# Kernel optimization log

Hardware: AMD Instinct MI355X
Metric: run time of the kernel (lower is better)

The kernel has to match this reference:

```python
import jax, jax.numpy as jnp
import numpy as np

DIM = 1024
DIM_HEADS = 128   # dim_inner
HEADS = 8         # dim_out // dim_heads
DHEAD = DIM_HEADS // HEADS  # = 16, per the Rearrange '(qkv h d)'
EPS = 1e-6


def setup_inputs() -> dict:
    key = jax.random.key(0)
    k1, k2, k3 = jax.random.split(key, 3)
    x = jax.random.normal(k1, (8, 4096, DIM), dtype=jnp.float32)
    norm_weight = jnp.ones((DIM,), dtype=jnp.float32)
    w_qkv = jax.random.normal(k2, (3 * DIM_HEADS, DIM), dtype=jnp.float32) * (1.0 / np.sqrt(DIM))
    temperature = jnp.zeros((HEADS, 1, 1), dtype=jnp.float32)
    w_out = jax.random.normal(k3, (DIM, DIM_HEADS), dtype=jnp.float32) * (1.0 / np.sqrt(DIM_HEADS))
    return {"x": x, "norm_weight": norm_weight, "w_qkv": w_qkv,
            "temperature": temperature, "w_out": w_out}


def _l2norm(t, axis=-1):
    # F.normalize(p=2): divide by max(||t||, eps) with eps=1e-12
    n = jnp.sqrt(jnp.sum(t * t, axis=axis, keepdims=True))
    return t / jnp.maximum(n, 1e-12)


def reference(x, norm_weight, w_qkv, temperature, w_out):
    b, n, _ = x.shape
    # RMSNorm
    ms = jnp.mean(x * x, axis=-1, keepdims=True)
    xn = x * jax.lax.rsqrt(ms + EPS) * norm_weight
    # QKV projection: b n (3 h d) -> 3 b h d n
    qkv = jnp.einsum('bnc,oc->bno', xn, w_qkv)
    qkv = qkv.reshape(b, n, 3, HEADS, DHEAD).transpose(2, 0, 3, 4, 1)  # [3,b,h,d,n]
    q, k, v = qkv[0], qkv[1], qkv[2]
    # l2-normalize along token axis (last axis, n)
    q = _l2norm(q)
    k = _l2norm(k)
    q = q * jnp.exp(temperature)  # (h,1,1) broadcasts over (b,h,d,n)
    # XCiT channel (cross-covariance) attention: d x d similarity over tokens
    sim = jnp.einsum('bhin,bhjn->bhij', q, k)
    attn = jax.nn.softmax(sim, axis=-1)
    out = jnp.einsum('bhij,bhjn->bhin', attn, v)  # [b,h,d,n]
    # b h d n -> b n (h d), then output projection
    out = out.transpose(0, 3, 1, 2).reshape(b, n, HEADS * DHEAD)
    return jnp.einsum('bnc,oc->bno', out, w_out)
```

## Files before the change

### kernel.cpp

```cpp
#include <hip/hip_runtime.h>
#include <hip/hip_bf16.h>
#include <stdint.h>

typedef __bf16 bf16_t;
typedef __bf16 bf16x8 __attribute__((ext_vector_type(8)));
typedef float  f32x4  __attribute__((ext_vector_type(4)));

#define DIM    1024
#define NTOK   4096
#define NB     8
#define ROWS   (NB*NTOK)
#define QKVC   384
#define INNER  128

#define GLD16(g, l) __builtin_amdgcn_global_load_lds( \
    (const __attribute__((address_space(1))) void*)(g), \
    (__attribute__((address_space(3))) void*)(l), 16, 0, 0)

#define OFF_WQ    131072u
#define OFF_QKV   1048576u
#define OFF_STATS 26214400u
#define OFF_ATTN  30932992u
#define OFF_WEFF  30998528u

__global__ __launch_bounds__(256) void k_wconv(const float* __restrict__ wq,
    const float* __restrict__ nw, bf16_t* __restrict__ wqb)
{
    int o = blockIdx.x;
    int c = threadIdx.x * 4;
    float4 wv = *reinterpret_cast<const float4*>(wq + (size_t)o*DIM + c);
    float4 nv = *reinterpret_cast<const float4*>(nw + c);
    bf16_t* dst = wqb + (size_t)o*DIM + c;
    dst[0]=(bf16_t)(wv.x*nv.x); dst[1]=(bf16_t)(wv.y*nv.y);
    dst[2]=(bf16_t)(wv.z*nv.z); dst[3]=(bf16_t)(wv.w*nv.w);
}

__global__ __launch_bounds__(512, 2) void k_qkv_gemm(const float* __restrict__ x,
    const bf16_t* __restrict__ wqb, bf16_t* __restrict__ qkv,
    float* __restrict__ stats)
{
    __shared__ bf16_t Al[2][128*64];
    __shared__ bf16_t Bl[2][384*64];
    __shared__ float srow[128];
    int mt = blockIdx.x;
    int row0 = mt*128;
    int t = threadIdx.x;
    int lane = t & 63, lr = lane & 15, lg = lane >> 4;
    int w = t >> 6, wm = w >> 2, wn = w & 3;

    int rA = t >> 2;
    int fo = (t & 3) * 16;
    const float* xrow = x + (size_t)(row0 + rA)*DIM + fo;
    int ws0 = ((t & 3)*2)     ^ (rA & 7);
    int ws1 = ((t & 3)*2 + 1) ^ (rA & 7);

    int srB = t >> 3;
    int sk8 = ((t & 7) ^ (srB & 7)) * 8;
    const bf16_t* bbase = wqb + (size_t)srB*DIM + sk8;
    int ldsoff = (t & ~63) * 8;

    int rsw = lr & 7;

    float4 u0, u1, u2, u3;

#define LOADA(kt) do {                                                   \
        const float4* _xs = reinterpret_cast<const float4*>(xrow + (kt)*64); \
        u0 = _xs[0]; u1 = _xs[1]; u2 = _xs[2]; u3 = _xs[3];              \
    } while (0)

#define STAGEB(buf, kt) do {                                             \
        int _ko = (kt)*64;                                               \
        _Pragma("unroll")                                                \
        for (int _c = 0; _c < 6; _c++)                                   \
            GLD16(bbase + _ko + (size_t)(64*_c)*DIM,                     \
                  &Bl[buf][ldsoff + _c*4096]);                           \
    } while (0)

#define WRITEA(buf) do {                                                 \
        ssq += u0.x*u0.x + u0.y*u0.y + u0.z*u0.z + u0.w*u0.w             \
             + u1.x*u1.x + u1.y*u1.y + u1.z*u1.z + u1.w*u1.w             \
             + u2.x*u2.x + u2.y*u2.y + u2.z*u2.z + u2.w*u2.w             \
             + u3.x*u3.x + u3.y*u3.y + u3.z*u3.z + u3.w*u3.w;            \
        bf16x8 v0, v1;                                                   \
        v0[0]=(bf16_t)u0.x; v0[1]=(bf16_t)u0.y; v0[2]=(bf16_t)u0.z;      \
        v0[3]=(bf16_t)u0.w; v0[4]=(bf16_t)u1.x; v0[5]=(bf16_t)u1.y;      \
        v0[6]=(bf16_t)u1.z; v0[7]=(bf16_t)u1.w;                          \
        v1[0]=(bf16_t)u2.x; v1[1]=(bf16_t)u2.y; v1[2]=(bf16_t)u2.z;      \
        v1[3]=(bf16_t)u2.w; v1[4]=(bf16_t)u3.x; v1[5]=(bf16_t)u3.y;      \
        v1[6]=(bf16_t)u3.z; v1[7]=(bf16_t)u3.w;                          \
        *reinterpret_cast<bf16x8*>(&Al[buf][rA*64 + ws0*8]) = v0;        \
        *reinterpret_cast<bf16x8*>(&Al[buf][rA*64 + ws1*8]) = v1;        \
    } while (0)

    float ssq = 0.f;
    f32x4 acc[4][6] = {};

    LOADA(0);
    STAGEB(0, 0);
    WRITEA(0);
    __syncthreads();

    for (int kt = 0; kt < 16; kt++) {
        int cur = kt & 1;
        if (kt < 15) {
            LOADA(kt + 1);
            STAGEB(cur ^ 1, kt + 1);
        }
        #pragma unroll
        for (int kk = 0; kk < 2; kk++) {
            int kb = ((kk*4 + lg) ^ rsw) * 8;
            bf16x8 af[4], bfr[6];
            #pragma unroll
            for (int mi = 0; mi < 4; mi++)
                af[mi] = *reinterpret_cast<const bf16x8*>(
                    &Al[cur][(wm*64 + mi*16 + lr)*64 + kb]);
            #pragma unroll
            for (int ni = 0; ni < 6; ni++)
                bfr[ni] = *reinterpret_cast<const bf16x8*>(
                    &Bl[cur][(wn*96 + ni*16 + lr)*64 + kb]);
            #pragma unroll
            for (int mi = 0; mi < 4; mi++)
                #pragma unroll
                for (int ni = 0; ni < 6; ni++)
                    acc[mi][ni] = __builtin_amdgcn_mfma_f32_16x16x32_bf16(
                        af[mi], bfr[ni], acc[mi][ni], 0, 0, 0);
        }
        if (kt < 15) WRITEA(cur ^ 1);
        __syncthreads();
    }
#undef LOADA
#undef STAGEB
#undef WRITEA

    ssq += __shfl_xor(ssq, 1, 64);
    ssq += __shfl_xor(ssq, 2, 64);
    if ((t & 3) == 0) srow[rA] = rsqrtf(ssq*(1.0f/DIM) + 1e-6f);
    __syncthreads();

    bf16_t* qk = &Bl[0][0];
    #pragma unroll
    for (int mi = 0; mi < 4; mi++)
        #pragma unroll
        for (int ni = 0; ni < 6; ni++) {
            int col_g = wn*96 + ni*16 + lr;
            #pragma unroll
            for (int rr = 0; rr < 4; rr++) {
                int rloc = wm*64 + mi*16 + lg*4 + rr;
                bf16_t val = (bf16_t)(acc[mi][ni][rr] * srow[rloc]);
                if (wn*96 + ni*16 >= 256)
                    qkv[(size_t)(row0 + rloc)*QKVC + col_g] = val;
                else
                    qk[rloc*256 + col_g] = val;
            }
        }
    __syncthreads();

    {
        int h = w;
        f32x4 g = {};
        #pragma unroll
        for (int ks = 0; ks < 4; ks++) {
            bf16x8 afr, bfr2;
            #pragma unroll
            for (int e = 0; e < 8; e++) {
                int tt = ks*32 + lg*8 + e;
                afr[e]  = qk[tt*256 + h*16 + lr];
                bfr2[e] = qk[tt*256 + 128 + h*16 + lr];
            }
            g = __builtin_amdgcn_mfma_f32_16x16x32_bf16(afr, bfr2, g, 0, 0, 0);
        }
        float* base = stats + ((size_t)mt*8 + h)*288;
        #pragma unroll
        for (int reg = 0; reg < 4; reg++)
            base[(lg*4 + reg)*16 + lr] = g[reg];
        float qs = 0.f, ks2 = 0.f;
        #pragma unroll
        for (int e = 0; e < 32; e++) {
            int tt = lg*32 + e;
            float qv = (float)qk[tt*256 + h*16 + lr];
            float kv = (float)qk[tt*256 + 128 + h*16 + lr];
            qs += qv*qv; ks2 += kv*kv;
        }
        qs  += __shfl_xor(qs, 16, 64);  qs  += __shfl_xor(qs, 32, 64);
        ks2 += __shfl_xor(ks2, 16, 64); ks2 += __shfl_xor(ks2, 32, 64);
        if (lane < 16) { base[256 + lr] = qs; base[272 + lr] = ks2; }
    }
}

__global__ __launch_bounds__(256) void k_attn(const float* __restrict__ stats,
    const float* __restrict__ temp, float* __restrict__ attn)
{
    int bid = blockIdx.x;
    int b = bid >> 3, h = bid & 7;
    int t = threadIdx.x, i = t >> 4, j = t & 15;
    float gsum = 0.f, qs = 0.f, ks = 0.f;
    for (int ch = 0; ch < 32; ch++) {
        const float* base = stats + ((size_t)(b*32 + ch)*8 + h)*288;
        gsum += base[i*16 + j];
        qs   += base[256 + i];
        ks   += base[272 + j];
    }
    float et  = expf(temp[h]);
    float sim = gsum * et / (fmaxf(sqrtf(qs), 1e-12f) * fmaxf(sqrtf(ks), 1e-12f));
    float m = sim;
    #pragma unroll
    for (int d = 1; d < 16; d <<= 1) m = fmaxf(m, __shfl_xor(m, d, 16));
    float e = expf(sim - m);
    float ssum = e;
    #pragma unroll
    for (int d = 1; d < 16; d <<= 1) ssum += __shfl_xor(ssum, d, 16);
    attn[((size_t)(b*8 + h)*16 + i)*16 + j] = e / ssum;
}

__global__ __launch_bounds__(256) void k_weff(const float* __restrict__ attn,
    const float* __restrict__ wout, bf16_t* __restrict__ weff)
{
    __shared__ float at[2048];
    int bid = blockIdx.x;
    int b = bid >> 5, ob = (bid & 31)*32;
    int t = threadIdx.x;
    #pragma unroll
    for (int r = 0; r < 8; r++) at[t + 256*r] = attn[(size_t)b*2048 + t + 256*r];
    __syncthreads();
    int c = t & 127, h = c >> 4, j = c & 15, oo = (t >> 7)*16;
    #pragma unroll
    for (int m = 0; m < 16; m++) {
        int o = ob + oo + m;
        float acc = 0.f;
        #pragma unroll
        for (int i2 = 0; i2 < 16; i2++)
            acc += wout[(size_t)o*INNER + h*16 + i2] * at[(h*16 + i2)*16 + j];
        weff[((size_t)b*DIM + o)*INNER + c] = (bf16_t)acc;
    }
}

__global__ __launch_bounds__(256) void k_out_gemm(const bf16_t* __restrict__ qkv,
    const bf16_t* __restrict__ weff, float* __restrict__ out)
{
    __shared__ bf16_t Al[128*136];
    __shared__ bf16_t Bl[128*136];
    int bid = blockIdx.x;
    int b = bid >> 8, rem = bid & 255;
    int mt = rem >> 3, nt = rem & 7;
    int tok0 = mt*128, o0 = nt*128;
    int t = threadIdx.x;
    #pragma unroll
    for (int rd = 0; rd < 8; rd++) {
        int r  = (t >> 4) + 16*rd;
        int c8 = (t & 15) * 8;
        *reinterpret_cast<uint4*>(&Al[r*136 + c8]) =
            *reinterpret_cast<const uint4*>(
                qkv + ((size_t)b*NTOK + tok0 + r)*QKVC + 256 + c8);
        *reinterpret_cast<uint4*>(&Bl[r*136 + c8]) =
            *reinterpret_cast<const uint4*>(
                weff + ((size_t)b*DIM + o0 + r)*INNER + c8);
    }
    __syncthreads();
    int w = t >> 6, lane = t & 63, lr = lane & 15, lg = lane >> 4;
    int wr = (w & 1)*64, wc = (w >> 1)*64;
    f32x4 acc[4][4] = {};
    #pragma unroll
    for (int kk = 0; kk < 4; kk++) {
        int kb = kk*32 + lg*8;
        bf16x8 af[4], bfr[4];
        #pragma unroll
        for (int mi = 0; mi < 4; mi++)
            af[mi] = *reinterpret_cast<const bf16x8*>(&Al[(wr + mi*16 + lr)*136 + kb]);
        #pragma unroll
        for (int ni = 0; ni < 4; ni++)
            bfr[ni] = *reinterpret_cast<const bf16x8*>(&Bl[(wc + ni*16 + lr)*136 + kb]);
        #pragma unroll
        for (int mi = 0; mi < 4; mi++)
            #pragma unroll
            for (int ni = 0; ni < 4; ni++)
                acc[mi][ni] = __builtin_amdgcn_mfma_f32_16x16x32_bf16(
                    af[mi], bfr[ni], acc[mi][ni], 0, 0, 0);
    }
    #pragma unroll
    for (int mi = 0; mi < 4; mi++)
        #pragma unroll
        for (int ni = 0; ni < 4; ni++) {
            int col_g = o0 + wc + ni*16 + lr;
            #pragma unroll
            for (int r = 0; r < 4; r++) {
                int row_g = tok0 + wr + mi*16 + lg*4 + r;
                out[((size_t)b*NTOK + row_g)*DIM + col_g] = acc[mi][ni][r];
            }
        }
}

extern "C" void kernel_launch(void* const* d_in, const int* in_sizes, int n_in,
                              void* d_out, int out_size, void* d_ws, size_t ws_size,
                              hipStream_t stream)
{
    const float* x    = (const float*)d_in[0];
    const float* nw   = (const float*)d_in[1];
    const float* wq   = (const float*)d_in[2];
    const float* temp = (const float*)d_in[3];
    const float* wout = (const float*)d_in[4];
    float* out = (float*)d_out;

    char* ws = (char*)d_ws;
    bf16_t* wqb   = (bf16_t*)(ws + OFF_WQ);
    bf16_t* qkv   = (bf16_t*)(ws + OFF_QKV);
    float*  stats = (float*)(ws + OFF_STATS);
    float*  attn  = (float*)(ws + OFF_ATTN);
    bf16_t* weff  = (bf16_t*)(ws + OFF_WEFF);

    k_wconv    <<<384,  256, 0, stream>>>(wq, nw, wqb);
    k_qkv_gemm <<<256,  512, 0, stream>>>(x, wqb, qkv, stats);
    k_attn     <<<64,   256, 0, stream>>>(stats, temp, attn);
    k_weff     <<<256,  256, 0, stream>>>(attn, wout, weff);
    k_out_gemm <<<2048, 256, 0, stream>>>(qkv, weff, out);
}
```

Measured before the change: 102.0 us.

## Prefetch x tiles two steps ahead with manual waitcnt and scheduling barriers

Restructures the QKV GEMM main loop so the fp32 x tile is loaded into registers two k-steps ahead, using two alternating register sets and a 2x-unrolled loop. Explicit s_waitcnt vmcnt/lgkmcnt, sched_barrier and raw s_barrier replace __syncthreads, so only the B LDS-direct loads are waited on before each barrier. The aim is to hide global-load latency for the A operand behind the MFMA work. The cost is extra VGPR pressure from the second register set, which could lower occupancy, and fragile hand-counted wait counts.

```diff
diff --git a/kernel.cpp b/kernel.cpp
--- a/kernel.cpp
+++ b/kernel.cpp
@@ -16,6 +16,9 @@
 #define GLD16(g, l) __builtin_amdgcn_global_load_lds( \
     (const __attribute__((address_space(1))) void*)(g), \
     (__attribute__((address_space(3))) void*)(l), 16, 0, 0)
+
+#define VMCNT(n) asm volatile("s_waitcnt vmcnt(" #n ")" ::: "memory")
+#define SBAR0()  __builtin_amdgcn_sched_barrier(0)
 
 #define OFF_WQ    131072u
 #define OFF_QKV   1048576u
@@ -61,11 +64,12 @@
 
     int rsw = lr & 7;
 
-    float4 u0, u1, u2, u3;
-
-#define LOADA(kt) do {                                                   \
+    float4 sa0, sa1, sa2, sa3;
+    float4 sb0, sb1, sb2, sb3;
+
+#define LOADA_(r0, r1, r2, r3, kt) do {                                  \
         const float4* _xs = reinterpret_cast<const float4*>(xrow + (kt)*64); \
-        u0 = _xs[0]; u1 = _xs[1]; u2 = _xs[2]; u3 = _xs[3];              \
+        r0 = _xs[0]; r1 = _xs[1]; r2 = _xs[2]; r3 = _xs[3];              \
     } while (0)
 
 #define STAGEB(buf, kt) do {                                             \
@@ -76,61 +80,80 @@
                   &Bl[buf][ldsoff + _c*4096]);                           \
     } while (0)
 
-#define WRITEA(buf) do {                                                 \
-        ssq += u0.x*u0.x + u0.y*u0.y + u0.z*u0.z + u0.w*u0.w             \
-             + u1.x*u1.x + u1.y*u1.y + u1.z*u1.z + u1.w*u1.w             \
-             + u2.x*u2.x + u2.y*u2.y + u2.z*u2.z + u2.w*u2.w             \
-             + u3.x*u3.x + u3.y*u3.y + u3.z*u3.z + u3.w*u3.w;            \
-        bf16x8 v0, v1;                                                   \
-        v0[0]=(bf16_t)u0.x; v0[1]=(bf16_t)u0.y; v0[2]=(bf16_t)u0.z;      \
-        v0[3]=(bf16_t)u0.w; v0[4]=(bf16_t)u1.x; v0[5]=(bf16_t)u1.y;      \
-        v0[6]=(bf16_t)u1.z; v0[7]=(bf16_t)u1.w;                          \
-        v1[0]=(bf16_t)u2.x; v1[1]=(bf16_t)u2.y; v1[2]=(bf16_t)u2.z;      \
-        v1[3]=(bf16_t)u2.w; v1[4]=(bf16_t)u3.x; v1[5]=(bf16_t)u3.y;      \
-        v1[6]=(bf16_t)u3.z; v1[7]=(bf16_t)u3.w;                          \
-        *reinterpret_cast<bf16x8*>(&Al[buf][rA*64 + ws0*8]) = v0;        \
-        *reinterpret_cast<bf16x8*>(&Al[buf][rA*64 + ws1*8]) = v1;        \
+#define WRITEA_(r0, r1, r2, r3, buf) do {                                \
+        ssq += r0.x*r0.x + r0.y*r0.y + r0.z*r0.z + r0.w*r0.w             \
+             + r1.x*r1.x + r1.y*r1.y + r1.z*r1.z + r1.w*r1.w             \
+             + r2.x*r2.x + r2.y*r2.y + r2.z*r2.z + r2.w*r2.w             \
+             + r3.x*r3.x + r3.y*r3.y + r3.z*r3.z + r3.w*r3.w;            \
+        bf16x8 _v0, _v1;                                                 \
+        _v0[0]=(bf16_t)r0.x; _v0[1]=(bf16_t)r0.y; _v0[2]=(bf16_t)r0.z;   \
+        _v0[3]=(bf16_t)r0.w; _v0[4]=(bf16_t)r1.x; _v0[5]=(bf16_t)r1.y;   \
+        _v0[6]=(bf16_t)r1.z; _v0[7]=(bf16_t)r1.w;                        \
+        _v1[0]=(bf16_t)r2.x; _v1[1]=(bf16_t)r2.y; _v1[2]=(bf16_t)r2.z;   \
+        _v1[3]=(bf16_t)r2.w; _v1[4]=(bf16_t)r3.x; _v1[5]=(bf16_t)r3.y;   \
+        _v1[6]=(bf16_t)r3.z; _v1[7]=(bf16_t)r3.w;                        \
+        *reinterpret_cast<bf16x8*>(&Al[buf][rA*64 + ws0*8]) = _v0;       \
+        *reinterpret_cast<bf16x8*>(&Al[buf][rA*64 + ws1*8]) = _v1;       \
+    } while (0)
+
+#define COMPUTE(CUR) do {                                                \
+        _Pragma("unroll")                                                \
+        for (int kk = 0; kk < 2; kk++) {                                 \
+            int kb = ((kk*4 + lg) ^ rsw) * 8;                            \
+            bf16x8 af[4], bfr[6];                                        \
+            _Pragma("unroll")                                            \
+            for (int mi = 0; mi < 4; mi++)                               \
+                af[mi] = *reinterpret_cast<const bf16x8*>(               \
+                    &Al[CUR][(wm*64 + mi*16 + lr)*64 + kb]);             \
+            _Pragma("unroll")                                            \
+            for (int ni = 0; ni < 6; ni++)                               \
+                bfr[ni] = *reinterpret_cast<const bf16x8*>(              \
+                    &Bl[CUR][(wn*96 + ni*16 + lr)*64 + kb]);             \
+            _Pragma("unroll")                                            \
+            for (int mi = 0; mi < 4; mi++)                               \
+                _Pragma("unroll")                                        \
+                for (int ni = 0; ni < 6; ni++)                           \
+                    acc[mi][ni] = __builtin_amdgcn_mfma_f32_16x16x32_bf16( \
+                        af[mi], bfr[ni], acc[mi][ni], 0, 0, 0);          \
+        }                                                                \
+    } while (0)
+
+#define STEP(kt, CUR, L0, L1, L2, L3, W0, W1, W2, W3) do {               \
+        if ((kt) + 1 < 16) STAGEB((CUR)^1, (kt)+1);                      \
+        SBAR0();                                                         \
+        if ((kt) + 2 < 16) LOADA_(L0, L1, L2, L3, (kt)+2);               \
+        SBAR0();                                                         \
+        COMPUTE(CUR);                                                    \
+        if ((kt) + 1 < 16) {                                             \
+            WRITEA_(W0, W1, W2, W3, (CUR)^1);     \
+            if ((kt) + 2 < 16) VMCNT(4); else VMCNT(0);                  \
+            SBAR0();                                                     \
+            asm volatile("s_waitcnt lgkmcnt(0)" ::: "memory");           \
+        }                                                                \
+        __builtin_amdgcn_s_barrier();                                    \
     } while (0)
 
     float ssq = 0.f;
     f32x4 acc[4][6] = {};
 
-    LOADA(0);
     STAGEB(0, 0);
-    WRITEA(0);
-    __syncthreads();
-
-    for (int kt = 0; kt < 16; kt++) {
-        int cur = kt & 1;
-        if (kt < 15) {
-            LOADA(kt + 1);
-            STAGEB(cur ^ 1, kt + 1);
-        }
-        #pragma unroll
-        for (int kk = 0; kk < 2; kk++) {
-            int kb = ((kk*4 + lg) ^ rsw) * 8;
-            bf16x8 af[4], bfr[6];
-            #pragma unroll
-            for (int mi = 0; mi < 4; mi++)
-                af[mi] = *reinterpret_cast<const bf16x8*>(
-                    &Al[cur][(wm*64 + mi*16 + lr)*64 + kb]);
-            #pragma unroll
-            for (int ni = 0; ni < 6; ni++)
-                bfr[ni] = *reinterpret_cast<const bf16x8*>(
-                    &Bl[cur][(wn*96 + ni*16 + lr)*64 + kb]);
-            #pragma unroll
-            for (int mi = 0; mi < 4; mi++)
-                #pragma unroll
-                for (int ni = 0; ni < 6; ni++)
-                    acc[mi][ni] = __builtin_amdgcn_mfma_f32_16x16x32_bf16(
-                        af[mi], bfr[ni], acc[mi][ni], 0, 0, 0);
-        }
-        if (kt < 15) WRITEA(cur ^ 1);
-        __syncthreads();
-    }
-#undef LOADA
+    SBAR0();
+    LOADA_(sa0, sa1, sa2, sa3, 0);
+    LOADA_(sb0, sb1, sb2, sb3, 1);
+    SBAR0();
+    WRITEA_(sa0, sa1, sa2, sa3, 0);
+    asm volatile("s_waitcnt lgkmcnt(0)" ::: "memory");
+    __builtin_amdgcn_s_barrier();
+
+    for (int kt2 = 0; kt2 < 16; kt2 += 2) {
+        STEP(kt2,     0, sa0, sa1, sa2, sa3, sb0, sb1, sb2, sb3);
+        STEP(kt2 + 1, 1, sb0, sb1, sb2, sb3, sa0, sa1, sa2, sa3);
+    }
+#undef LOADA_
 #undef STAGEB
-#undef WRITEA
+#undef WRITEA_
+#undef COMPUTE
+#undef STEP
 
     ssq += __shfl_xor(ssq, 1, 64);
     ssq += __shfl_xor(ssq, 2, 64);
```

Result: no change. 102.4 us (+0.3%).
